# Kernel optimization log

Measured on AMD Instinct MI355X. Metric: run time of the kernel, lower is better.

Reference implementation:

```python
import jax, jax.numpy as jnp
import numpy as np


def _dwconv_silu(feat, w, b):
    # feat: (B, L, C); depthwise 1D conv, kernel 7, pad 3, then SiLU (PointLiteConv)
    x = jnp.swapaxes(feat, 1, 2)  # (B, C, L)
    y = jax.lax.conv_general_dilated(x, w, (1,), [(3, 3)],
                                     feature_group_count=x.shape[1],
                                     dimension_numbers=('NCH', 'OIH', 'NCH'))
    y = y + b[None, :, None]
    return jnp.swapaxes(jax.nn.silu(y), 1, 2)


def _issm_scan(x, h0, dt, A, Bm, Cm, Dp):
    # x: (B,L,H,P)  h0: (B,H,P,N)  dt: (B,L,H,N)  A: (H,1)  Bm,Cm: (B,L,1,N)  Dp: (H,)
    dA = jnp.exp(dt * A)                      # (B,L,H,N) discrete decay
    u = dt * Bm                               # (B,L,H,N) input coeff (ngroups=1 broadcast)
    Cb = jnp.broadcast_to(Cm, dt.shape)       # (B,L,H,N)

    def step(h, inp):
        dA_t, u_t, x_t, c_t = inp             # (B,H,N),(B,H,N),(B,H,P),(B,H,N)
        h = dA_t[:, :, None, :] * h + x_t[..., None] * u_t[:, :, None, :]
        return h, jnp.einsum('bhpn,bhn->bhp', h, c_t)

    xs = tuple(jnp.moveaxis(a, 1, 0) for a in (dA, u, x, Cb))
    hF, ys = jax.lax.scan(step, h0, xs)
    y = jnp.moveaxis(ys, 0, 1) + Dp[None, None, :, None] * x
    return y, hF


def setup_inputs() -> dict:
    key = jax.random.key(0)
    ks = jax.random.split(key, 20)
    B, L, K = 2, 2048, 64
    d_model, d_state, d_dist, H, G, d_inner = 512, 64, 4, 8, 1, 1024
    c_conv = d_inner + 2 * G  # 1026
    s = 0.02
    dt0 = jnp.exp(jax.random.uniform(ks[12], (H,)) * (np.log(0.1) - np.log(1e-4)) + np.log(1e-4))
    dt0 = jnp.clip(dt0, 1e-4, None)
    return {
        'in_key': jax.random.normal(ks[0], (B, L, d_model), jnp.float32),
        'in_query': jax.random.normal(ks[1], (B, K, d_model), jnp.float32),
        'dist': jax.random.uniform(ks[2], (B, L, K, d_dist), jnp.float32),
        'key_xyz': jax.random.normal(ks[3], (B, L, 3), jnp.float32),
        'key_proj_w': jax.random.normal(ks[4], (2 * d_inner + 2 * G + H, d_model), jnp.float32) * s,
        'key_conv_w': jax.random.normal(ks[5], (c_conv, 1, 7), jnp.float32) * s,
        'key_conv_b': jnp.zeros((c_conv,), jnp.float32),
        'key_conv_back_w': jax.random.normal(ks[6], (c_conv, 1, 7), jnp.float32) * s,
        'key_conv_back_b': jnp.zeros((c_conv,), jnp.float32),
        'query_proj_w': jax.random.normal(ks[7], (d_inner, d_model), jnp.float32) * s,
        'bc_proj_w': jax.random.normal(ks[8], (2 * G, d_dist), jnp.float32) * s,
        'dt_proj_w': jax.random.normal(ks[9], (H, d_dist), jnp.float32) * s,
        'dt_bias': dt0 + jnp.log(-jnp.expm1(-dt0)),
        'A_log': jnp.log(jax.random.uniform(ks[10], (H,), jnp.float32, 1.0, 16.0)),
        'D_param': jnp.ones((H,), jnp.float32),
        'out_key_w': jax.random.normal(ks[11], (d_model, d_inner), jnp.float32) * s,
        'out_query_w': jax.random.normal(ks[13], (d_model, d_inner), jnp.float32) * s,
        'key_norm_w': jnp.ones((d_inner,), jnp.float32),
        'q_ln_w': jnp.ones((d_inner,), jnp.float32),
        'q_ln_b': jnp.zeros((d_inner,), jnp.float32),
    }


def reference(in_key, in_query, dist, key_xyz, key_proj_w, key_conv_w, key_conv_b,
              key_conv_back_w, key_conv_back_b, query_proj_w, bc_proj_w, dt_proj_w,
              dt_bias, A_log, D_param, out_key_w, out_query_w, key_norm_w, q_ln_w, q_ln_b):
    B, L, _ = in_key.shape
    K = in_query.shape[1]
    d_inner = query_proj_w.shape[0]
    H = dt_bias.shape[0]
    G = bc_proj_w.shape[0] // 2
    P = d_inner // H

    zxbcdt = in_key @ key_proj_w.T                       # (B,L,2*di+2G+H)
    z = zxbcdt[..., :d_inner]
    xbc = zxbcdt[..., d_inner:2 * d_inner + 2 * G]
    dt_head = zxbcdt[..., 2 * d_inner + 2 * G:]          # (B,L,H)

    xbc_f = _dwconv_silu(xbc, key_conv_w, key_conv_b)
    x = xbc_f[..., :d_inner]
    b_bias = xbc_f[..., d_inner:d_inner + G]
    c_bias = xbc_f[..., d_inner + G:]
    xbc_b = _dwconv_silu(xbc, key_conv_back_w, key_conv_back_b)
    x_bk = xbc_b[..., :d_inner]
    b_bias_b = xbc_b[..., d_inner:d_inner + G]
    c_bias_b = xbc_b[..., d_inner + G:]

    # initial state: 'b l (h hd) -> b h hd l'  -> (B,H,P,K)
    h0 = (in_query @ query_proj_w.T).reshape(B, K, H, P).transpose(0, 2, 3, 1)
    A = -jnp.exp(A_log)[:, None]                         # (H,1), repeated over d_state

    bc = dist @ bc_proj_w.T                              # (B,L,K,2G)
    b_base = jnp.swapaxes(bc[..., :G], -1, -2)           # (B,L,G,K)
    c_base = jnp.swapaxes(bc[..., G:], -1, -2)
    Bm = b_base + b_bias[..., None]
    Cm = c_base + c_bias[..., None]
    Bmb = b_base + b_bias_b[..., None]
    Cmb = c_base + c_bias_b[..., None]

    dt = jax.nn.softplus(jnp.swapaxes(dist @ dt_proj_w.T, -1, -2)
                         + dt_head[..., None] + dt_bias[None, None, :, None])  # (B,L,H,K)

    xh = x.reshape(B, L, H, P)
    y_f, h_f = _issm_scan(xh, h0, dt, A, Bm, Cm, D_param)
    xb = jnp.flip(x_bk.reshape(B, L, H, P), 1)
    y_b, h_b = _issm_scan(xb, h0, jnp.flip(dt, 1), A, jnp.flip(Bmb, 1), jnp.flip(Cmb, 1), D_param)
    y = (y_f + jnp.flip(y_b, 1)) * 0.5                   # (B,L,H,P)
    h_last = (h_f + h_b) * 0.5                           # (B,H,P,K)

    key_feat = y.reshape(B, L, d_inner)
    xg = key_feat * jax.nn.silu(z)                       # gated RMSNorm (gate before norm)
    key_n = xg * jax.lax.rsqrt(jnp.mean(xg * xg, -1, keepdims=True) + 1e-5) * key_norm_w
    out_key = key_n @ out_key_w.T

    q = h_last.transpose(0, 3, 1, 2).reshape(B, K, d_inner)  # 'b h p l -> b l (h p)'
    mu = jnp.mean(q, -1, keepdims=True)
    var = jnp.mean((q - mu) ** 2, -1, keepdims=True)
    qn = (q - mu) * jax.lax.rsqrt(var + 1e-5) * q_ln_w + q_ln_b
    out_query = qn @ out_query_w.T
    return out_key, out_query
```

## Files before the change

kernel.cpp:

```cpp
#include <hip/hip_runtime.h>
#include <hip/hip_bf16.h>
#include <cstdint>

constexpr int B_ = 2, L_ = 2048, K_ = 64, H_ = 8, P_ = 128, DI = 1024;
constexpr int NPROJ = 2058;
constexpr int NC = L_ / 64;
constexpr int XBCS = 1040;

typedef unsigned short u16;
typedef short bf16x8 __attribute__((ext_vector_type(8)));
typedef float f32x4 __attribute__((ext_vector_type(4)));

__constant__ int c_sz[20] = {2097152,65536,1048576,12288,1053696,7182,1026,7182,1026,
                             524288,8,32,8,8,8,524288,524288,1024,1024,1024};
__constant__ int c_of[20] = {16,2097168,2162704,3211280,3223568,4277264,4284446,4285472,
                             4292654,4293680,4817968,4817976,4818008,4818016,4818024,
                             4818032,5342320,5866608,5867632,5868656};
constexpr int TOT_IN = 5869664;
constexpr int OF_INKEY = 16, OF_INQ = 2097168, OF_DIST = 2162704, OF_KPW = 3223568;
constexpr int OF_CONVW = 4277264, OF_CONVB = 4284446, OF_CONVBW = 4285472, OF_CONVBB = 4292654;
constexpr int OF_QPW = 4293680, OF_BCW = 4817968, OF_DTW = 4817976, OF_DTBIAS = 4818008;
constexpr int OF_ALOG = 4818016, OF_D = 4818024, OF_OKW = 4818032, OF_OQW = 5342320;
constexpr int OF_KNW = 5866608, OF_QLW = 5867632, OF_QLB = 5868656;
constexpr int SEG_A = 2097152, SEG_W = 2176*512, SEG_O = 524288;
// ... 33 lines not shown
    uint2 u = *(const uint2*)p;
    float4 r;
    r.x = __uint_as_float(u.x << 16);
    r.y = __uint_as_float(u.x & 0xffff0000u);
    r.z = __uint_as_float(u.y << 16);
    r.w = __uint_as_float(u.y & 0xffff0000u);
    return r;
}
DEV float4 b2f4u(uint2 u) {
    float4 r;
    r.x = __uint_as_float(u.x << 16);
    r.y = __uint_as_float(u.x & 0xffff0000u);
    r.z = __uint_as_float(u.y << 16);
    r.w = __uint_as_float(u.y & 0xffff0000u);
    return r;
}
DEV uint2 pku2(float4 v) {
    uint2 u;
    u.x = (unsigned)f2b(v.x) | ((unsigned)f2b(v.y) << 16);
    u.y = (unsigned)f2b(v.z) | ((unsigned)f2b(v.w) << 16);
    return u;
}
DEV void st4b(u16* p, float4 v) { *(uint2*)p = pku2(v); }
DEV unsigned pk2(float a, float b) { return (unsigned)f2b(a) | ((unsigned)f2b(b) << 16); }

#define GLL16(gp, lp) __builtin_amdgcn_global_load_lds( \
    (const __attribute__((address_space(1))) unsigned int*)(gp), \
    (__attribute__((address_space(3))) unsigned int*)(lp), 16, 0, 0)

struct SrcPtrs { const void* p[20]; };

__global__ void k_sentinel(float* out) { out[threadIdx.x] = 1e9f; }

DEV u16 cvt_elem(const void* p, int idx, bool bf) {
    if (bf) return ((const u16*)p)[idx];
    return f2b(((const float*)p)[idx]);
}
__global__ __launch_bounds__(256) void k_stage(SrcPtrs sp, float* ws) {
    int g = blockIdx.x * 256 + threadIdx.x;
    bool bf = (((const u16*)sp.p[17])[0] == 0x3F80u);
    if (g < TOT_IN) {
        int seg = 0, rem = g;
        while (rem >= c_sz[seg]) { rem -= c_sz[seg]; ++seg; }
        if (seg == 0 || seg == 1 || seg == 4 || seg == 9 || seg == 15 || seg == 16) return;
        float v;
        if (bf) v = b2f(((const u16*)sp.p[seg])[rem]);
        else    v = ((const float*)sp.p[seg])[rem];
// ... 37 lines not shown
    #pragma unroll
    for (int i = 0; i < 4; ++i)
        #pragma unroll
        for (int j = 0; j < 4; ++j) acc[i][j] = zero4;
    for (int kt = 0; kt < 512; kt += 32) {
        __syncthreads();
        GLL16(Ab + (size_t)(m0 + srow)*512      + kt + scol, As + (w*512));
        GLL16(Ab + (size_t)(m0 + 64 + srow)*512 + kt + scol, As + (2048 + w*512));
        GLL16(Wb + (size_t)(n0 + srow)*512      + kt + scol, Bs + (w*512));
        GLL16(Wb + (size_t)(n0 + 64 + srow)*512 + kt + scol, Bs + (2048 + w*512));
        __syncthreads();
        bf16x8 af[4], bfr[4];
        #pragma unroll
        for (int mi = 0; mi < 4; ++mi) af[mi]  = *(const bf16x8*)&As[(wm*64 + mi*16 + lr)*32 + lq*8];
        #pragma unroll
        for (int ni = 0; ni < 4; ++ni) bfr[ni] = *(const bf16x8*)&Bs[(wn*64 + ni*16 + lr)*32 + lq*8];
        #pragma unroll
        for (int mi = 0; mi < 4; ++mi)
            #pragma unroll
            for (int ni = 0; ni < 4; ++ni)
                acc[mi][ni] = __builtin_amdgcn_mfma_f32_16x16x32_bf16(af[mi], bfr[ni], acc[mi][ni], 0, 0, 0);
    }
    u16* xbc = (u16*)(ws + WXBC);
    #pragma unroll
    for (int mi = 0; mi < 4; ++mi)
        #pragma unroll
        for (int ni = 0; ni < 4; ++ni)
            #pragma unroll
            for (int r = 0; r < 4; ++r) {
                int m = m0 + wm*64 + mi*16 + lq*4 + r;
                int n = n0 + wn*64 + ni*16 + lr;
                if (n >= NPROJ) continue;
                float v = acc[mi][ni][r];
                if (n < 1024)       ws[WZ + m*1024 + n] = v;
                else if (n < 2050)  xbc[m*XBCS + (n-1024)] = f2b(v);
                else                ws[WDTH + m*8 + (n-2050)] = v;
            }
}

__global__ __launch_bounds__(256) void k_conv(float* ws) {
    int tile = blockIdx.x;
    int bl0 = tile * 16;
    int l0 = bl0 & (L_ - 1);
    int base = bl0 - l0;
    int cb = blockIdx.y, tid = threadIdx.x;
    int cch = cb * 256 + tid;
    if (cb == 4) { if (tid >= 2) return; cch = 1024 + tid; }
    const u16* xbc = (const u16*)(ws + WXBC);
    const float* wfp = ws + OF_CONVW + cch*7;
    const float* wbp = ws + OF_CONVBW + cch*7;
    float wf[7], wb[7];
    #pragma unroll
    for (int j = 0; j < 7; ++j) { wf[j] = wfp[j]; wb[j] = wbp[j]; }
    float bfv = ws[OF_CONVB + cch], bbv = ws[OF_CONVBB + cch];
    float win[22];
    #pragma unroll
    for (int j = 0; j < 22; ++j) {
        int l2 = l0 - 3 + j;
        win[j] = (l2 >= 0 && l2 < L_) ? b2f(xbc[(base + l2)*XBCS + cch]) : 0.f;
    }
    u16* XF = (u16*)(ws + WXF);
    u16* XB = (u16*)(ws + WXBK);
    #pragma unroll
    for (int i = 0; i < 16; ++i) {
        float af = bfv, ab = bbv;
        #pragma unroll
        for (int j = 0; j < 7; ++j) { af += win[i+j]*wf[j]; ab += win[i+j]*wb[j]; }
        af = silu_(af); ab = silu_(ab);
        if (cb < 4) {
            XF[(bl0 + i)*1024 + cch] = f2b(af);
            XB[(bl0 + i)*1024 + cch] = f2b(ab);
        } else if (cch == 1024) {
            ws[WBBF + bl0 + i] = af; ws[WBBB + bl0 + i] = ab;
        } else {
            ws[WCBF + bl0 + i] = af; ws[WCBB + bl0 + i] = ab;
        }
    }
}

__global__ __launch_bounds__(256) void k_dtbc(float* ws) {
    int g = blockIdx.x * 256 + threadIdx.x;
    if (g >= B_*L_*K_) return;
    int k = g & 63, bl = g >> 6;
    float4 d4 = ld4(&ws[OF_DIST + g*4]);
    const float* bcw = ws + OF_BCW;
    ws[WBBASE + g] = d4.x*bcw[0] + d4.y*bcw[1] + d4.z*bcw[2] + d4.w*bcw[3];
    ws[WCBASE + g] = d4.x*bcw[4] + d4.y*bcw[5] + d4.z*bcw[6] + d4.w*bcw[7];
    const float* dtw = ws + OF_DTW;
    const float* dtb = ws + OF_DTBIAS;
    const float* dth = ws + WDTH + bl*8;
    #pragma unroll
    for (int h = 0; h < 8; ++h) {
        float t = d4.x*dtw[h*4] + d4.y*dtw[h*4+1] + d4.z*dtw[h*4+2] + d4.w*dtw[h*4+3]
                + dth[h] + dtb[h];
        float sp = (t > 20.f) ? t : log1pf(__expf(t));
        ws[WDT + (bl*8 + h)*64 + k] = sp;
    }
}

__global__ __launch_bounds__(256) void k_h0mm(float* ws) {
    __shared__ u16 As[128*32], Bs[128*32];
    const u16* Ab = (const u16*)(ws + OF_INQ);
    const u16* Wb = (const u16*)(ws + OF_QPW);
    int tid = threadIdx.x, w = tid >> 6, l = tid & 63;
    int n0 = blockIdx.x * 128;
    int wm = w & 1, wn = w >> 1;
    int lr = l & 15, lq = l >> 4;
    int srow = tid >> 2, scol = (tid & 3) * 8;
    f32x4 zero4 = {0.f, 0.f, 0.f, 0.f};
    f32x4 acc[4][4];
    #pragma unroll
    for (int i = 0; i < 4; ++i)
        #pragma unroll
        for (int j = 0; j < 4; ++j) acc[i][j] = zero4;
    for (int kt = 0; kt < 512; kt += 32) {
        __syncthreads();
        GLL16(Ab + (size_t)(srow)*512      + kt + scol, As + (w*512));
        GLL16(Ab + (size_t)(64 + srow)*512 + kt + scol, As + (2048 + w*512));
        GLL16(Wb + (size_t)(n0 + srow)*512      + kt + scol, Bs + (w*512));
        GLL16(Wb + (size_t)(n0 + 64 + srow)*512 + kt + scol, Bs + (2048 + w*512));
        __syncthreads();
        bf16x8 af[4], bfr[4];
        #pragma unroll
        for (int mi = 0; mi < 4; ++mi) af[mi]  = *(const bf16x8*)&As[(wm*64 + mi*16 + lr)*32 + lq*8];
        #pragma unroll
        for (int ni = 0; ni < 4; ++ni) bfr[ni] = *(const bf16x8*)&Bs[(wn*64 + ni*16 + lr)*32 + lq*8];
        #pragma unroll
        for (int mi = 0; mi < 4; ++mi)
            #pragma unroll
            for (int ni = 0; ni < 4; ++ni)
                acc[mi][ni] = __builtin_amdgcn_mfma_f32_16x16x32_bf16(af[mi], bfr[ni], acc[mi][ni], 0, 0, 0);
    }
    #pragma unroll
    for (int mi = 0; mi < 4; ++mi)
        #pragma unroll
        for (int ni = 0; ni < 4; ++ni)
            #pragma unroll
            for (int r = 0; r < 4; ++r) {
                int m = wm*64 + mi*16 + lq*4 + r;
                int n = n0 + wn*64 + ni*16 + lr;
                int b = m >> 6, kq = m & 63, h = n >> 7, p = n & 127;
                ws[WH0I + ((b*8 + h)*64 + kq)*128 + p] = acc[mi][ni][r];
            }
}

__global__ __launch_bounds__(256, 3) void k_scanA(float* ws) {
    __shared__ float scs[4096];
    __shared__ u16 sUeD[64*72];
    __shared__ u16 sCe[64*72];
    __shared__ u16 sM[64*72];
    __shared__ u16 sUeO[32*72];
    __shared__ float sG[128];
    u16* sXt = (u16*)scs;
    int bx = blockIdx.x;
    int c = bx & 31, dir = (bx >> 5) & 1, h = (bx >> 6) & 7, b = bx >> 9;
    int tid = threadIdx.x, w = tid >> 6, l = tid & 63;
    int lr = l & 15, tq = l >> 4;
    float Ah = -__expf(ws[OF_ALOG + h]);
    float Dv = ws[OF_D + h];
    const float* dt = ws + WDT;
    const float* bbase = ws + WBBASE; const float* cbase = ws + WCBASE;
    const float* bbias = ws + (dir ? WBBB : WBBF);
    const float* cbias = ws + (dir ? WCBB : WCBF);
    for (int q = tid; q < 1024; q += 256) {
        int t = q >> 4, k4 = (q & 15) << 2;
        int gt = dir ? (L_ - 1 - (c*64 + t)) : (c*64 + t);
// ... 59 lines not shown
                bf16x8 a  = *(const bf16x8*)&sCe[(ttile*16 + lr)*72 + kh*32 + tq*8];
                bf16x8 bb = *(const bf16x8*)&Bb [(stile*16 + lr)*72 + kh*32 + tq*8];
                acc = __builtin_amdgcn_mfma_f32_16x16x32_bf16(a, bb, acc, 0, 0, 0);
            }
            #pragma unroll
            for (int r = 0; r < 4; ++r) {
                int row = ttile*16 + tq*4 + r, col = stile*16 + lr;
                sM[row*72 + col] = f2b(row >= col ? acc[r] : 0.f);
            }
        }
    }
    __syncthreads();
    for (int q = tid; q < 4096; q += 256) {
        int k = q >> 6, s = q & 63;
        sCe[k*72 + s] = f2b(b2f(sUeD[s*72 + k]) * sG[((s >> 5) << 6) + k]);
    }
    __syncthreads();
    bf16x8 aM[2], aU[2];
    #pragma unroll
    for (int kh = 0; kh < 2; ++kh) {
        aM[kh] = *(const bf16x8*)&sM [(w*16 + lr)*72 + kh*32 + tq*8];
        aU[kh] = *(const bf16x8*)&sCe[(w*16 + lr)*72 + kh*32 + tq*8];
    }
    float* yloc = ws + (dir ? WYB : WYF);
    const u16* Xsrc = (const u16*)(ws + (dir ? WXBK : WXF));
    u16* DH = (u16*)(ws + WDH);
    int bhd = (b*8 + h)*2 + dir;
    for (int ph = 0; ph < 2; ++ph) {
        #pragma unroll
        for (int g3 = 0; g3 < 2; ++g3) {
            int t0 = w*16 + g3*8;
            u16 x[8];
            #pragma unroll
            for (int j = 0; j < 8; ++j) {
                int row = c*64 + t0 + j;
                int gt = dir ? (L_ - 1 - row) : row;
                x[j] = Xsrc[(b*L_ + gt)*1024 + h*128 + ph*64 + l];
            }
            uint4 qv;
            qv.x = (unsigned)x[0] | ((unsigned)x[1] << 16);
            qv.y = (unsigned)x[2] | ((unsigned)x[3] << 16);
            qv.z = (unsigned)x[4] | ((unsigned)x[5] << 16);
            qv.w = (unsigned)x[6] | ((unsigned)x[7] << 16);
            *(uint4*)&sXt[l*72 + t0] = qv;
        }
        __syncthreads();
        f32x4 accY[4], accD[4];
        #pragma unroll
        for (int pi = 0; pi < 4; ++pi) { accY[pi] = {0.f,0.f,0.f,0.f}; accD[pi] = {0.f,0.f,0.f,0.f}; }
        #pragma unroll
        for (int pi = 0; pi < 4; ++pi) {
            bf16x8 bX0 = *(const bf16x8*)&sXt[(pi*16 + lr)*72 +  0 + tq*8];
            bf16x8 bX1 = *(const bf16x8*)&sXt[(pi*16 + lr)*72 + 32 + tq*8];
            accY[pi] = __builtin_amdgcn_mfma_f32_16x16x32_bf16(aM[0], bX0, accY[pi], 0, 0, 0);
            accY[pi] = __builtin_amdgcn_mfma_f32_16x16x32_bf16(aM[1], bX1, accY[pi], 0, 0, 0);
            accD[pi] = __builtin_amdgcn_mfma_f32_16x16x32_bf16(aU[0], bX0, accD[pi], 0, 0, 0);
            accD[pi] = __builtin_amdgcn_mfma_f32_16x16x32_bf16(aU[1], bX1, accD[pi], 0, 0, 0);
        }
        #pragma unroll
        for (int pi = 0; pi < 4; ++pi) {
            int p = pi*16 + lr;
            #pragma unroll
            for (int r = 0; r < 4; ++r) {
                int t = w*16 + tq*4 + r;
                int gt = dir ? (L_ - 1 - (c*64 + t)) : (c*64 + t);
                float xv = b2f(sXt[p*72 + t]);
                yloc[(b*L_ + gt)*1024 + h*128 + ph*64 + p] = accY[pi][r] + Dv*xv;
                int ks = w*16 + tq*4 + r;
                DH[(size_t)((bhd*32 + c)*64 + ks)*128 + ph*64 + p] = f2b(accD[pi][r]);
            }
        }
        __syncthreads();
    }
}

__global__ __launch_bounds__(256) void k_carry(float* ws) {
    int bx = blockIdx.x;
    int pg = bx & 7, dir = (bx >> 3) & 1, h = (bx >> 4) & 7, b = bx >> 7;
    int tid = threadIdx.x;
    int k = tid >> 2, p = pg*16 + (tid & 3)*4;
    int bhd = (b*8 + h)*2 + dir;
    float ear[NC];
    const float* Eb = ws + WE + bhd*32*64 + k;
    #pragma unroll
    for (int c = 0; c < NC; ++c) ear[c] = Eb[c*64];
    float4 hr = ld4(&ws[WH0I + ((b*8 + h)*64 + k)*128 + p]);
    u16* DH = (u16*)(ws + WDH);
    size_t base0 = (size_t)(bhd*32*64 + k)*128 + p;
    uint2 dbuf[4];
    #pragma unroll
    for (int i = 0; i < 4; ++i) dbuf[i] = *(const uint2*)&DH[base0 + (size_t)i*8192];
    #pragma unroll
    for (int c = 0; c < NC; ++c) {
        float4 d = b2f4u(dbuf[c & 3]);
        *(uint2*)&DH[base0 + (size_t)c*8192] = pku2(hr);
        if (c + 4 < NC) dbuf[c & 3] = *(const uint2*)&DH[base0 + (size_t)(c + 4)*8192];
        float e = ear[c];
        hr.x = e*hr.x + d.x; hr.y = e*hr.y + d.y; hr.z = e*hr.z + d.z; hr.w = e*hr.w + d.w;
    }
    st4(&ws[WHFIN + (bhd*64 + k)*128 + p], hr);
}

__global__ __launch_bounds__(256, 3) void k_scanB(float* ws) {
    __shared__ float scs[4096];
    __shared__ u16 sCf[64*72], sCb[64*72];
    __shared__ u16 sHf[64*72], sHb[64*72];
    int bx = blockIdx.x;
    int j = bx & 31, h = (bx >> 5) & 7, b = bx >> 8;
    int tid = threadIdx.x, w = tid >> 6, l = tid & 63;
    int lr = l & 15, tq = l >> 4;
    float Ah = -__expf(ws[OF_ALOG + h]);
    for (int q = tid; q < 1024; q += 256) {
        int t = q >> 4, k4 = (q & 15) << 2;
        int bl = b*L_ + j*64 + t;
        float4 dv = ld4(&ws[WDT + (bl*8 + h)*64 + k4]);
        st4(&scs[t*64 + k4], make_float4(dv.x*Ah, dv.y*Ah, dv.z*Ah, dv.w*Ah));
    }
    __syncthreads();
    {
        float* tmp = (float*)sCf;
        int kk = tid & 63, seg = tid >> 6;
        float run = 0.f;
        for (int t = seg*16; t < seg*16 + 16; ++t) { run += scs[t*64 + kk]; scs[t*64 + kk] = run; }
        tmp[seg*64 + kk] = run;
        __syncthreads();
        float off = 0.f;
        for (int s2 = 0; s2 < seg; ++s2) off += tmp[s2*64 + kk];
        __syncthreads();
        if (seg > 0)
            for (int t = seg*16; t < seg*16 + 16; ++t) scs[t*64 + kk] += off;
    }
    __syncthreads();
    for (int q = tid; q < 4096; q += 256) {
        int t = q >> 6, k = q & 63;
        int bl = b*L_ + j*64 + t;
        float pref = scs[t*64 + k];
        float prev = (t == 0) ? 0.f : scs[(t-1)*64 + k];
        float tot  = scs[63*64 + k];
        float cb0 = ws[WCBASE + bl*64 + k];
        sCf[t*72 + k] = f2b((cb0 + ws[WCBF + bl]) * __expf(pref));
        sCb[t*72 + k] = f2b((cb0 + ws[WCBB + bl]) * __expf(tot - prev));
    }
    const u16* h0f = (const u16*)(ws + WDH) + (size_t)((((b*8 + h)*2 + 0)*32 + j)*64)*128;
    const u16* h0b = (const u16*)(ws + WDH) + (size_t)((((b*8 + h)*2 + 1)*32 + (31 - j))*64)*128;
    __syncthreads();
    bf16x8 af[2], ab_[2];
    #pragma unroll
    for (int kh = 0; kh < 2; ++kh) {
        af[kh]  = *(const bf16x8*)&sCf[(w*16 + lr)*72 + kh*32 + tq*8];
        ab_[kh] = *(const bf16x8*)&sCb[(w*16 + lr)*72 + kh*32 + tq*8];
    }
    u16* xgb = (u16*)(ws + WXF);
    for (int ph = 0; ph < 2; ++ph) {
        #pragma unroll
        for (int g2 = 0; g2 < 2; ++g2) {
            int k0 = w*16 + g2*8;
            u16 xf[8], xb[8];
            #pragma unroll
            for (int jj = 0; jj < 8; ++jj) {
                xf[jj] = h0f[(k0 + jj)*128 + ph*64 + l];
                xb[jj] = h0b[(k0 + jj)*128 + ph*64 + l];
            }
            uint4 qf, qb;
            qf.x = (unsigned)xf[0] | ((unsigned)xf[1] << 16);
            qf.y = (unsigned)xf[2] | ((unsigned)xf[3] << 16);
            qf.z = (unsigned)xf[4] | ((unsigned)xf[5] << 16);
            qf.w = (unsigned)xf[6] | ((unsigned)xf[7] << 16);
            qb.x = (unsigned)xb[0] | ((unsigned)xb[1] << 16);
            qb.y = (unsigned)xb[2] | ((unsigned)xb[3] << 16);
            qb.z = (unsigned)xb[4] | ((unsigned)xb[5] << 16);
            qb.w = (unsigned)xb[6] | ((unsigned)xb[7] << 16);
            *(uint4*)&sHf[l*72 + k0] = qf;
            *(uint4*)&sHb[l*72 + k0] = qb;
        }
        __syncthreads();
        f32x4 accf[4], accb[4];
        #pragma unroll
        for (int pi = 0; pi < 4; ++pi) { accf[pi] = {0.f,0.f,0.f,0.f}; accb[pi] = {0.f,0.f,0.f,0.f}; }
        #pragma unroll
        for (int pi = 0; pi < 4; ++pi) {
            bf16x8 bf0 = *(const bf16x8*)&sHf[(pi*16 + lr)*72 +  0 + tq*8];
            bf16x8 bf1 = *(const bf16x8*)&sHf[(pi*16 + lr)*72 + 32 + tq*8];
            bf16x8 bb0 = *(const bf16x8*)&sHb[(pi*16 + lr)*72 +  0 + tq*8];
            bf16x8 bb1 = *(const bf16x8*)&sHb[(pi*16 + lr)*72 + 32 + tq*8];
            accf[pi] = __builtin_amdgcn_mfma_f32_16x16x32_bf16(af[0],  bf0, accf[pi], 0, 0, 0);
            accf[pi] = __builtin_amdgcn_mfma_f32_16x16x32_bf16(af[1],  bf1, accf[pi], 0, 0, 0);
            accb[pi] = __builtin_amdgcn_mfma_f32_16x16x32_bf16(ab_[0], bb0, accb[pi], 0, 0, 0);
            accb[pi] = __builtin_amdgcn_mfma_f32_16x16x32_bf16(ab_[1], bb1, accb[pi], 0, 0, 0);
        }
        #pragma unroll
        for (int pi = 0; pi < 4; ++pi) {
            int p = pi*16 + lr;
            #pragma unroll
            for (int r = 0; r < 4; ++r) {
                int t = w*16 + tq*4 + r;
                int off = (b*L_ + j*64 + t)*1024 + h*128 + ph*64 + p;
                float yf = ws[WYF + off], yb = ws[WYB + off], zv = ws[WZ + off];
                float o = 0.5f*(yf + yb + accf[pi][r] + accb[pi][r]) * silu_(zv);
                xgb[off] = f2b(o);
            }
        }
        __syncthreads();
    }
}

__global__ __launch_bounds__(256) void k_rms(float* ws) {
    __shared__ float red[4];
    __shared__ float sstat;
    int row = blockIdx.x;
    const u16* xg = (const u16*)(ws + WXF) + row*1024;
    float4 v = b2f4(&xg[threadIdx.x*4]);
    float ss = v.x*v.x + v.y*v.y + v.z*v.z + v.w*v.w;
    #pragma unroll
    for (int o = 32; o > 0; o >>= 1) ss += __shfl_down(ss, o);
    if ((threadIdx.x & 63) == 0) red[threadIdx.x >> 6] = ss;
    __syncthreads();
    if (threadIdx.x == 0) {
        float t = red[0] + red[1] + red[2] + red[3];
        sstat = rsqrtf(t * (1.f/1024.f) + 1e-5f);
    }
    __syncthreads();
    float sr = sstat;
    float4 kw = ld4(&ws[OF_KNW + threadIdx.x*4]);
// ... 27 lines not shown
        for (int ni = 0; ni < 2; ++ni) bfr[ni] = *(const bf16x8*)&Bs[(wn*32 + ni*16 + lr)*32 + lq*8];
        #pragma unroll
        for (int mi = 0; mi < 4; ++mi)
            #pragma unroll
            for (int ni = 0; ni < 2; ++ni)
                acc[mi][ni] = __builtin_amdgcn_mfma_f32_16x16x32_bf16(af[mi], bfr[ni], acc[mi][ni], 0, 0, 0);
    }
    bool bf = (((const u16*)in17)[0] == 0x3F80u);
    #pragma unroll
    for (int mi = 0; mi < 4; ++mi)
        #pragma unroll
        for (int ni = 0; ni < 2; ++ni)
            #pragma unroll
            for (int r = 0; r < 4; ++r) {
                int m = m0 + wm*64 + mi*16 + lq*4 + r;
                int n = n0 + wn*32 + ni*16 + lr;
                int idx = m*512 + n;
                float v = acc[mi][ni][r];
                if (bf) ((__hip_bfloat16*)d_out)[idx] = __float2bfloat16(v);
                else    ((float*)d_out)[idx] = v;
            }
}

__global__ __launch_bounds__(256) void k_queryLN(float* ws) {
    __shared__ float sq[1024];
    __shared__ float red1[4], red2[4], sstat[2];
    int bk = blockIdx.x;
    int b = bk >> 6, kq = bk & 63;
    int tid = threadIdx.x;
    for (int i = tid; i < 1024; i += 256) {
        int h = i >> 7, p = i & 127;
        int i0 = (((b*8 + h)*2 + 0)*64 + kq)*128 + p;
        int i1 = (((b*8 + h)*2 + 1)*64 + kq)*128 + p;
        sq[i] = 0.5f * (ws[WHFIN + i0] + ws[WHFIN + i1]);
    }
    __syncthreads();
    float4 v = ld4(&sq[tid*4]);
    float s1 = v.x + v.y + v.z + v.w;
    float s2 = v.x*v.x + v.y*v.y + v.z*v.z + v.w*v.w;
    #pragma unroll
    for (int o = 32; o > 0; o >>= 1) { s1 += __shfl_down(s1, o); s2 += __shfl_down(s2, o); }
    if ((tid & 63) == 0) { red1[tid >> 6] = s1; red2[tid >> 6] = s2; }
    __syncthreads();
    if (tid == 0) {
        float S1 = red1[0]+red1[1]+red1[2]+red1[3];
        float S2 = red2[0]+red2[1]+red2[2]+red2[3];
        float mu = S1 * (1.f/1024.f);
        float var = S2 * (1.f/1024.f) - mu*mu;
        sstat[0] = mu; sstat[1] = rsqrtf(var + 1e-5f);
    }
    __syncthreads();
    float mu = sstat[0], rs = sstat[1];
    u16* qn = (u16*)(ws + WXBC);
    float4 kw = ld4(&ws[OF_QLW + tid*4]);
    float4 kb = ld4(&ws[OF_QLB + tid*4]);
    st4b(qn + bk*1024 + tid*4,
         make_float4((v.x - mu)*rs*kw.x + kb.x, (v.y - mu)*rs*kw.y + kb.y,
                     (v.z - mu)*rs*kw.z + kb.z, (v.w - mu)*rs*kw.w + kb.w));
}

__global__ __launch_bounds__(256) void k_queryMM(float* ws, void* d_out, const void* in17) {
    __shared__ u16 As[128*32], Bs[128*32];
    const u16* Ab = (const u16*)(ws + WXBC);
    const u16* Wb = (const u16*)(ws + OF_OQW);
    int tid = threadIdx.x, w = tid >> 6, l = tid & 63;
    int n0 = blockIdx.x * 128;
    int wm = w & 1, wn = w >> 1;
    int lr = l & 15, lq = l >> 4;
    int srow = tid >> 2, scol = (tid & 3) * 8;
    f32x4 zero4 = {0.f, 0.f, 0.f, 0.f};
    f32x4 acc[4][4];
    #pragma unroll
    for (int i = 0; i < 4; ++i)
        #pragma unroll
        for (int jj = 0; jj < 4; ++jj) acc[i][jj] = zero4;
    for (int kt = 0; kt < 1024; kt += 32) {
        __syncthreads();
        GLL16(Ab + (size_t)(srow)*1024      + kt + scol, As + (w*512));
        GLL16(Ab + (size_t)(64 + srow)*1024 + kt + scol, As + (2048 + w*512));
        GLL16(Wb + (size_t)(n0 + srow)*1024      + kt + scol, Bs + (w*512));
        GLL16(Wb + (size_t)(n0 + 64 + srow)*1024 + kt + scol, Bs + (2048 + w*512));
        __syncthreads();
        bf16x8 af[4], bfr[4];
        #pragma unroll
        for (int mi = 0; mi < 4; ++mi) af[mi]  = *(const bf16x8*)&As[(wm*64 + mi*16 + lr)*32 + lq*8];
        #pragma unroll
        for (int ni = 0; ni < 4; ++ni) bfr[ni] = *(const bf16x8*)&Bs[(wn*64 + ni*16 + lr)*32 + lq*8];
        #pragma unroll
        for (int mi = 0; mi < 4; ++mi)
            #pragma unroll
            for (int ni = 0; ni < 4; ++ni)
                acc[mi][ni] = __builtin_amdgcn_mfma_f32_16x16x32_bf16(af[mi], bfr[ni], acc[mi][ni], 0, 0, 0);
    }
    bool bf = (((const u16*)in17)[0] == 0x3F80u);
    #pragma unroll
    for (int mi = 0; mi < 4; ++mi)
        #pragma unroll
        for (int ni = 0; ni < 4; ++ni)
            #pragma unroll
            for (int r = 0; r < 4; ++r) {
                int m = wm*64 + mi*16 + lq*4 + r;
                int n = n0 + wn*64 + ni*16 + lr;
                if (n >= 512) continue;
                int idx = 2097152 + m*512 + n;
                float v = acc[mi][ni][r];
                if (bf) ((__hip_bfloat16*)d_out)[idx] = __float2bfloat16(v);
                else    ((float*)d_out)[idx] = v;
            }
}

extern "C" void kernel_launch(void* const* d_in, const int* in_sizes, int n_in,
                              void* d_out, int out_size, void* d_ws, size_t ws_size,
                              hipStream_t stream) {
    float* ws = (float*)d_ws;
    if (ws_size < (size_t)WEND * sizeof(float)) {
        k_sentinel<<<1, 64, 0, stream>>>((float*)d_out);
        return;
    }
    SrcPtrs sp;
    for (int i = 0; i < 20; ++i) sp.p[i] = d_in[i];
    k_stage<<<(TOT_IN + NCAST + 255)/256, 256, 0, stream>>>(sp, ws);
    k_gemm_proj<<<dim3(17, 32), 256, 0, stream>>>(ws);
    k_conv<<<dim3(B_*L_/16, 5), 256, 0, stream>>>(ws);
    k_dtbc<<<(B_*L_*K_)/256, 256, 0, stream>>>(ws);
    k_h0mm<<<8, 256, 0, stream>>>(ws);
    k_scanA<<<1024, 256, 0, stream>>>(ws);
    k_carry<<<256, 256, 0, stream>>>(ws);
    k_scanB<<<512, 256, 0, stream>>>(ws);
    k_rms<<<4096, 256, 0, stream>>>(ws);
    k_outkey<<<dim3(8, 32), 256, 0, stream>>>(ws, d_out, d_in[17]);
    k_queryLN<<<128, 256, 0, stream>>>(ws);
    k_queryMM<<<4, 256, 0, stream>>>(ws, d_out, d_in[17]);
}
```

Measured before the change: 332.4 us.

## Fuse mid-stage kernels, store z and y as bf16, stage scan stores through LDS

Merges conv, dt/BC, and h0 GEMM into one launch. Folds the query LayerNorm and query GEMM into extra blocks of scanB. Stores z and the scan outputs as bf16 instead of fp32, which halves that traffic. Scan outputs and the gating epilogue now go through swizzled LDS so global stores and loads are 16-byte coalesced. This cuts launch count and memory traffic, at the cost of extra barriers and lower precision for the intermediates.

Result: slower. 362.4 us (+9.0%).

```diff
diff --git a/kernel.cpp b/kernel.cpp
--- a/kernel.cpp
+++ b/kernel.cpp
@@ -79,7 +79,6 @@
     return u;
 }
 DEV void st4b(u16* p, float4 v) { *(uint2*)p = pku2(v); }
-DEV unsigned pk2(float a, float b) { return (unsigned)f2b(a) | ((unsigned)f2b(b) << 16); }
 
 #define GLL16(gp, lp) __builtin_amdgcn_global_load_lds( \
     (const __attribute__((address_space(1))) unsigned int*)(gp), \
@@ -163,6 +162,7 @@
                 acc[mi][ni] = __builtin_amdgcn_mfma_f32_16x16x32_bf16(af[mi], bfr[ni], acc[mi][ni], 0, 0, 0);
     }
     u16* xbc = (u16*)(ws + WXBC);
+    u16* zb  = (u16*)(ws + WZ);
     #pragma unroll
     for (int mi = 0; mi < 4; ++mi)
         #pragma unroll
@@ -173,116 +173,117 @@
                 int n = n0 + wn*64 + ni*16 + lr;
                 if (n >= NPROJ) continue;
                 float v = acc[mi][ni][r];
-                if (n < 1024)       ws[WZ + m*1024 + n] = v;
+                if (n < 1024)       zb[m*1024 + n] = f2b(v);
                 else if (n < 2050)  xbc[m*XBCS + (n-1024)] = f2b(v);
                 else                ws[WDTH + m*8 + (n-2050)] = v;
             }
 }
 
-__global__ __launch_bounds__(256) void k_conv(float* ws) {
-    int tile = blockIdx.x;
-    int bl0 = tile * 16;
-    int l0 = bl0 & (L_ - 1);
-    int base = bl0 - l0;
-    int cb = blockIdx.y, tid = threadIdx.x;
-    int cch = cb * 256 + tid;
-    if (cb == 4) { if (tid >= 2) return; cch = 1024 + tid; }
-    const u16* xbc = (const u16*)(ws + WXBC);
-    const float* wfp = ws + OF_CONVW + cch*7;
-    const float* wbp = ws + OF_CONVBW + cch*7;
-    float wf[7], wb[7];
-    #pragma unroll
-    for (int j = 0; j < 7; ++j) { wf[j] = wfp[j]; wb[j] = wbp[j]; }
-    float bfv = ws[OF_CONVB + cch], bbv = ws[OF_CONVBB + cch];
-    float win[22];
-    #pragma unroll
-    for (int j = 0; j < 22; ++j) {
-        int l2 = l0 - 3 + j;
-        win[j] = (l2 >= 0 && l2 < L_) ? b2f(xbc[(base + l2)*XBCS + cch]) : 0.f;
-    }
-    u16* XF = (u16*)(ws + WXF);
-    u16* XB = (u16*)(ws + WXBK);
-    #pragma unroll
-    for (int i = 0; i < 16; ++i) {
-        float af = bfv, ab = bbv;
-        #pragma unroll
-        for (int j = 0; j < 7; ++j) { af += win[i+j]*wf[j]; ab += win[i+j]*wb[j]; }
-        af = silu_(af); ab = silu_(ab);
-        if (cb < 4) {
-            XF[(bl0 + i)*1024 + cch] = f2b(af);
-            XB[(bl0 + i)*1024 + cch] = f2b(ab);
-        } else if (cch == 1024) {
-            ws[WBBF + bl0 + i] = af; ws[WBBB + bl0 + i] = ab;
-        } else {
-            ws[WCBF + bl0 + i] = af; ws[WCBB + bl0 + i] = ab;
-        }
-    }
-}
-
-__global__ __launch_bounds__(256) void k_dtbc(float* ws) {
-    int g = blockIdx.x * 256 + threadIdx.x;
-    if (g >= B_*L_*K_) return;
-    int k = g & 63, bl = g >> 6;
-    float4 d4 = ld4(&ws[OF_DIST + g*4]);
-    const float* bcw = ws + OF_BCW;
-    ws[WBBASE + g] = d4.x*bcw[0] + d4.y*bcw[1] + d4.z*bcw[2] + d4.w*bcw[3];
-    ws[WCBASE + g] = d4.x*bcw[4] + d4.y*bcw[5] + d4.z*bcw[6] + d4.w*bcw[7];
-    const float* dtw = ws + OF_DTW;
-    const float* dtb = ws + OF_DTBIAS;
-    const float* dth = ws + WDTH + bl*8;
-    #pragma unroll
-    for (int h = 0; h < 8; ++h) {
-        float t = d4.x*dtw[h*4] + d4.y*dtw[h*4+1] + d4.z*dtw[h*4+2] + d4.w*dtw[h*4+3]
-                + dth[h] + dtb[h];
-        float sp = (t > 20.f) ? t : log1pf(__expf(t));
-        ws[WDT + (bl*8 + h)*64 + k] = sp;
-    }
-}
-
-__global__ __launch_bounds__(256) void k_h0mm(float* ws) {
+__global__ __launch_bounds__(256) void k_mid(float* ws) {
     __shared__ u16 As[128*32], Bs[128*32];
-    const u16* Ab = (const u16*)(ws + OF_INQ);
-    const u16* Wb = (const u16*)(ws + OF_QPW);
-    int tid = threadIdx.x, w = tid >> 6, l = tid & 63;
-    int n0 = blockIdx.x * 128;
-    int wm = w & 1, wn = w >> 1;
-    int lr = l & 15, lq = l >> 4;
-    int srow = tid >> 2, scol = (tid & 3) * 8;
-    f32x4 zero4 = {0.f, 0.f, 0.f, 0.f};
-    f32x4 acc[4][4];
-    #pragma unroll
-    for (int i = 0; i < 4; ++i)
-        #pragma unroll
-        for (int j = 0; j < 4; ++j) acc[i][j] = zero4;
-    for (int kt = 0; kt < 512; kt += 32) {
-        __syncthreads();
-        GLL16(Ab + (size_t)(srow)*512      + kt + scol, As + (w*512));
-        GLL16(Ab + (size_t)(64 + srow)*512 + kt + scol, As + (2048 + w*512));
-        GLL16(Wb + (size_t)(n0 + srow)*512      + kt + scol, Bs + (w*512));
-        GLL16(Wb + (size_t)(n0 + 64 + srow)*512 + kt + scol, Bs + (2048 + w*512));
-        __syncthreads();
-        bf16x8 af[4], bfr[4];
-        #pragma unroll
-        for (int mi = 0; mi < 4; ++mi) af[mi]  = *(const bf16x8*)&As[(wm*64 + mi*16 + lr)*32 + lq*8];
-        #pragma unroll
-        for (int ni = 0; ni < 4; ++ni) bfr[ni] = *(const bf16x8*)&Bs[(wn*64 + ni*16 + lr)*32 + lq*8];
+    int bx = blockIdx.x, tid = threadIdx.x;
+    if (bx < 1280) {
+        int cb = bx >> 8, tile = bx & 255;
+        int bl0 = tile * 16;
+        int l0 = bl0 & (L_ - 1);
+        int base = bl0 - l0;
+        int cch = cb * 256 + tid;
+        if (cb == 4) { if (tid >= 2) return; cch = 1024 + tid; }
+        const u16* xbc = (const u16*)(ws + WXBC);
+        const float* wfp = ws + OF_CONVW + cch*7;
+        const float* wbp = ws + OF_CONVBW + cch*7;
+        float wf[7], wb[7];
+        #pragma unroll
+        for (int j = 0; j < 7; ++j) { wf[j] = wfp[j]; wb[j] = wbp[j]; }
+        float bfv = ws[OF_CONVB + cch], bbv = ws[OF_CONVBB + cch];
+        float win[22];
+        #pragma unroll
+        for (int j = 0; j < 22; ++j) {
+            int l2 = l0 - 3 + j;
+            win[j] = (l2 >= 0 && l2 < L_) ? b2f(xbc[(base + l2)*XBCS + cch]) : 0.f;
+        }
+        u16* XF = (u16*)(ws + WXF);
+        u16* XB = (u16*)(ws + WXBK);
+        #pragma unroll
+        for (int i = 0; i < 16; ++i) {
+            float af = bfv, ab = bbv;
+            #pragma unroll
+            for (int j = 0; j < 7; ++j) { af += win[i+j]*wf[j]; ab += win[i+j]*wb[j]; }
+            af = silu_(af); ab = silu_(ab);
+            if (cb < 4) {
+                XF[(bl0 + i)*1024 + cch] = f2b(af);
+                XB[(bl0 + i)*1024 + cch] = f2b(ab);
+            } else if (cch == 1024) {
+                ws[WBBF + bl0 + i] = af; ws[WBBB + bl0 + i] = ab;
+            } else {
+                ws[WCBF + bl0 + i] = af; ws[WCBB + bl0 + i] = ab;
+            }
+        }
+        return;
+    }
+    if (bx < 2304) {
+        int g = (bx - 1280) * 256 + tid;
+        int k = g & 63, bl = g >> 6;
+        float4 d4 = ld4(&ws[OF_DIST + g*4]);
+        const float* bcw = ws + OF_BCW;
+        ws[WBBASE + g] = d4.x*bcw[0] + d4.y*bcw[1] + d4.z*bcw[2] + d4.w*bcw[3];
+        ws[WCBASE + g] = d4.x*bcw[4] + d4.y*bcw[5] + d4.z*bcw[6] + d4.w*bcw[7];
+        const float* dtw = ws + OF_DTW;
+        const float* dtb = ws + OF_DTBIAS;
+        const float* dth = ws + WDTH + bl*8;
+        #pragma unroll
+        for (int h = 0; h < 8; ++h) {
+            float t = d4.x*dtw[h*4] + d4.y*dtw[h*4+1] + d4.z*dtw[h*4+2] + d4.w*dtw[h*4+3]
+                    + dth[h] + dtb[h];
+            float sp = (t > 20.f) ? t : log1pf(__expf(t));
+            ws[WDT + (bl*8 + h)*64 + k] = sp;
+        }
+        return;
+    }
+    {
+        const u16* Ab = (const u16*)(ws + OF_INQ);
+        const u16* Wb = (const u16*)(ws + OF_QPW);
+        int w = tid >> 6, l = tid & 63;
+        int n0 = (bx - 2304) * 128;
+        int wm = w & 1, wn = w >> 1;
+        int lr = l & 15, lq = l >> 4;
+        int srow = tid >> 2, scol = (tid & 3) * 8;
+        f32x4 zero4 = {0.f, 0.f, 0.f, 0.f};
+        f32x4 acc[4][4];
+        #pragma unroll
+        for (int i = 0; i < 4; ++i)
+            #pragma unroll
+            for (int j = 0; j < 4; ++j) acc[i][j] = zero4;
+        for (int kt = 0; kt < 512; kt += 32) {
+            __syncthreads();
+            GLL16(Ab + (size_t)(srow)*512      + kt + scol, As + (w*512));
+            GLL16(Ab + (size_t)(64 + srow)*512 + kt + scol, As + (2048 + w*512));
+            GLL16(Wb + (size_t)(n0 + srow)*512      + kt + scol, Bs + (w*512));
+            GLL16(Wb + (size_t)(n0 + 64 + srow)*512 + kt + scol, Bs + (2048 + w*512));
+            __syncthreads();
+            bf16x8 af[4], bfr[4];
+            #pragma unroll
+            for (int mi = 0; mi < 4; ++mi) af[mi]  = *(const bf16x8*)&As[(wm*64 + mi*16 + lr)*32 + lq*8];
+            #pragma unroll
+            for (int ni = 0; ni < 4; ++ni) bfr[ni] = *(const bf16x8*)&Bs[(wn*64 + ni*16 + lr)*32 + lq*8];
+            #pragma unroll
+            for (int mi = 0; mi < 4; ++mi)
+                #pragma unroll
+                for (int ni = 0; ni < 4; ++ni)
+                    acc[mi][ni] = __builtin_amdgcn_mfma_f32_16x16x32_bf16(af[mi], bfr[ni], acc[mi][ni], 0, 0, 0);
+        }
         #pragma unroll
         for (int mi = 0; mi < 4; ++mi)
             #pragma unroll
             for (int ni = 0; ni < 4; ++ni)
-                acc[mi][ni] = __builtin_amdgcn_mfma_f32_16x16x32_bf16(af[mi], bfr[ni], acc[mi][ni], 0, 0, 0);
-    }
-    #pragma unroll
-    for (int mi = 0; mi < 4; ++mi)
-        #pragma unroll
-        for (int ni = 0; ni < 4; ++ni)
-            #pragma unroll
-            for (int r = 0; r < 4; ++r) {
-                int m = wm*64 + mi*16 + lq*4 + r;
-                int n = n0 + wn*64 + ni*16 + lr;
-                int b = m >> 6, kq = m & 63, h = n >> 7, p = n & 127;
-                ws[WH0I + ((b*8 + h)*64 + kq)*128 + p] = acc[mi][ni][r];
-            }
+                #pragma unroll
+                for (int r = 0; r < 4; ++r) {
+                    int m = wm*64 + mi*16 + lq*4 + r;
+                    int n = n0 + wn*64 + ni*16 + lr;
+                    int b = m >> 6, kq = m & 63, h = n >> 7, p = n & 127;
+                    ws[WH0I + ((b*8 + h)*64 + kq)*128 + p] = acc[mi][ni][r];
+                }
+    }
 }
 
 __global__ __launch_bounds__(256, 3) void k_scanA(float* ws) {
@@ -388,7 +389,10 @@
         aM[kh] = *(const bf16x8*)&sM [(w*16 + lr)*72 + kh*32 + tq*8];
         aU[kh] = *(const bf16x8*)&sCe[(w*16 + lr)*72 + kh*32 + tq*8];
     }
-    float* yloc = ws + (dir ? WYB : WYF);
+    __syncthreads();
+    u16* sYst = sM;
+    u16* sDst = sCe;
+    u16* yloc16 = (u16*)(ws + (dir ? WYB : WYF));
     const u16* Xsrc = (const u16*)(ws + (dir ? WXBK : WXF));
     u16* DH = (u16*)(ws + WDH);
     int bhd = (b*8 + h)*2 + dir;
@@ -429,12 +433,26 @@
             #pragma unroll
             for (int r = 0; r < 4; ++r) {
                 int t = w*16 + tq*4 + r;
-                int gt = dir ? (L_ - 1 - (c*64 + t)) : (c*64 + t);
                 float xv = b2f(sXt[p*72 + t]);
-                yloc[(b*L_ + gt)*1024 + h*128 + ph*64 + p] = accY[pi][r] + Dv*xv;
-                int ks = w*16 + tq*4 + r;
-                DH[(size_t)((bhd*32 + c)*64 + ks)*128 + ph*64 + p] = f2b(accD[pi][r]);
-            }
+                sYst[t*64 + (((pi + t) & 3) << 4) + lr] = f2b(accY[pi][r] + Dv*xv);
+                sDst[t*64 + (((pi + t) & 3) << 4) + lr] = f2b(accD[pi][r]);
+            }
+        }
+        __syncthreads();
+        {
+            int t2 = tid >> 2, cg = tid & 3;
+            int swz = ((cg + t2) & 3) << 4;
+            int gt2 = dir ? (L_ - 1 - (c*64 + t2)) : (c*64 + t2);
+            uint4 y0 = *(uint4*)&sYst[t2*64 + swz];
+            uint4 d0 = *(uint4*)&sDst[t2*64 + swz];
+            u16* yp = yloc16 + (size_t)(b*L_ + gt2)*1024 + h*128 + ph*64 + cg*16;
+            u16* dp = DH + (size_t)((bhd*32 + c)*64 + t2)*128 + ph*64 + cg*16;
+            *(uint4*)yp = y0;
+            *(uint4*)dp = d0;
+            uint4 y1 = *(uint4*)&sYst[t2*64 + swz + 8];
+            uint4 d1 = *(uint4*)&sDst[t2*64 + swz + 8];
+            *(uint4*)(yp + 8) = y1;
+            *(uint4*)(dp + 8) = d1;
         }
         __syncthreads();
     }
@@ -467,13 +485,108 @@
     st4(&ws[WHFIN + (bhd*64 + k)*128 + p], hr);
 }
 
-__global__ __launch_bounds__(256, 3) void k_scanB(float* ws) {
+__global__ __launch_bounds__(256, 3) void k_scanB(float* ws, void* d_out, const void* in17) {
     __shared__ float scs[4096];
     __shared__ u16 sCf[64*72], sCb[64*72];
     __shared__ u16 sHf[64*72], sHb[64*72];
     int bx = blockIdx.x;
+    int tid = threadIdx.x;
+    bool bf16out = (((const u16*)in17)[0] == 0x3F80u);
+    if (bx >= 512) {
+        int n0 = (bx - 512) * 128;
+        u16* As = (u16*)scs;
+        u16* Bs = (u16*)scs + 4096;
+        float* smu = (float*)sCf;
+        float* srs = smu + 128;
+        {
+            int m = tid >> 1, halfsel = tid & 1;
+            int b = m >> 6, kq = m & 63;
+            float s1 = 0.f, s2 = 0.f;
+            for (int i = halfsel*512; i < halfsel*512 + 512; i += 4) {
+                int h2 = i >> 7, p = i & 127;
+                float4 hf = ld4(&ws[WHFIN + ((((b*8 + h2)*2 + 0)*64 + kq)*128 + p)]);
+                float4 hb = ld4(&ws[WHFIN + ((((b*8 + h2)*2 + 1)*64 + kq)*128 + p)]);
+                float qx = 0.5f*(hf.x+hb.x), qy = 0.5f*(hf.y+hb.y);
+                float qz = 0.5f*(hf.z+hb.z), qw = 0.5f*(hf.w+hb.w);
+                s1 += qx+qy+qz+qw;
+                s2 += qx*qx+qy*qy+qz*qz+qw*qw;
+            }
+            s1 += __shfl_xor(s1, 1); s2 += __shfl_xor(s2, 1);
+            if (halfsel == 0) {
+                float mu = s1 * (1.f/1024.f);
+                float var = s2 * (1.f/1024.f) - mu*mu;
+                smu[m] = mu; srs[m] = rsqrtf(var + 1e-5f);
+            }
+        }
+        __syncthreads();
+        const u16* Wb = (const u16*)(ws + OF_OQW);
+        int w = tid >> 6, l = tid & 63;
+        int wm = w & 1, wn = w >> 1, lr = l & 15, lq = l >> 4;
+        int srow = tid >> 2, scol = (tid & 3) * 8;
+        f32x4 acc[4][4];
+        #pragma unroll
+        for (int i = 0; i < 4; ++i)
+            #pragma unroll
+            for (int j = 0; j < 4; ++j) acc[i][j] = {0.f,0.f,0.f,0.f};
+        int m2 = tid >> 1, csel = (tid & 1) * 16;
+        int b2 = m2 >> 6, kq2 = m2 & 63;
+        float mu2 = smu[m2], rs2 = srs[m2];
+        for (int kt = 0; kt < 1024; kt += 32) {
+            __syncthreads();
+            GLL16(Wb + (size_t)(n0 + srow)*1024      + kt + scol, Bs + (w*512));
+            GLL16(Wb + (size_t)(n0 + 64 + srow)*1024 + kt + scol, Bs + (2048 + w*512));
+            {
+                int i0 = kt + csel;
+                int h2 = i0 >> 7, p0 = i0 & 127;
+                const float* hfp = ws + WHFIN + ((((b2*8 + h2)*2 + 0)*64 + kq2)*128 + p0);
+                const float* hbp = ws + WHFIN + ((((b2*8 + h2)*2 + 1)*64 + kq2)*128 + p0);
+                uint2 pk[4];
+                #pragma unroll
+                for (int j4 = 0; j4 < 4; ++j4) {
+                    float4 hf = ld4(hfp + j4*4);
+                    float4 hb = ld4(hbp + j4*4);
+                    float4 kw = ld4(&ws[OF_QLW + i0 + j4*4]);
+                    float4 kb = ld4(&ws[OF_QLB + i0 + j4*4]);
+                    float4 qn;
+                    qn.x = (0.5f*(hf.x+hb.x) - mu2)*rs2*kw.x + kb.x;
+                    qn.y = (0.5f*(hf.y+hb.y) - mu2)*rs2*kw.y + kb.y;
+                    qn.z = (0.5f*(hf.z+hb.z) - mu2)*rs2*kw.z + kb.z;
+                    qn.w = (0.5f*(hf.w+hb.w) - mu2)*rs2*kw.w + kb.w;
+                    pk[j4] = pku2(qn);
+                }
+                *(uint4*)&As[m2*32 + csel]     = make_uint4(pk[0].x, pk[0].y, pk[1].x, pk[1].y);
+                *(uint4*)&As[m2*32 + csel + 8] = make_uint4(pk[2].x, pk[2].y, pk[3].x, pk[3].y);
+            }
+            __syncthreads();
+            bf16x8 af[4], bfr[4];
+            #pragma unroll
+            for (int mi = 0; mi < 4; ++mi) af[mi]  = *(const bf16x8*)&As[(wm*64 + mi*16 + lr)*32 + lq*8];
+            #pragma unroll
+            for (int ni = 0; ni < 4; ++ni) bfr[ni] = *(const bf16x8*)&Bs[(wn*64 + ni*16 + lr)*32 + lq*8];
+            #pragma unroll
+            for (int mi = 0; mi < 4; ++mi)
+                #pragma unroll
+                for (int ni = 0; ni < 4; ++ni)
+                    acc[mi][ni] = __builtin_amdgcn_mfma_f32_16x16x32_bf16(af[mi], bfr[ni], acc[mi][ni], 0, 0, 0);
+        }
+        #pragma unroll
+        for (int mi = 0; mi < 4; ++mi)
+            #pragma unroll
+            for (int ni = 0; ni < 4; ++ni)
+                #pragma unroll
+                for (int r = 0; r < 4; ++r) {
+                    int m = wm*64 + mi*16 + lq*4 + r;
+                    int n = n0 + wn*64 + ni*16 + lr;
+                    if (n >= 512) continue;
+                    int idx = 2097152 + m*512 + n;
+                    float v = acc[mi][ni][r];
+                    if (bf16out) ((__hip_bfloat16*)d_out)[idx] = __float2bfloat16(v);
+                    else         ((float*)d_out)[idx] = v;
+                }
+        return;
+    }
     int j = bx & 31, h = (bx >> 5) & 7, b = bx >> 8;
-    int tid = threadIdx.x, w = tid >> 6, l = tid & 63;
+    int w = tid >> 6, l = tid & 63;
     int lr = l & 15, tq = l >> 4;
     float Ah = -__expf(ws[OF_ALOG + h]);
     for (int q = tid; q < 1024; q += 256) {
@@ -516,7 +629,14 @@
         af[kh]  = *(const bf16x8*)&sCf[(w*16 + lr)*72 + kh*32 + tq*8];
         ab_[kh] = *(const bf16x8*)&sCb[(w*16 + lr)*72 + kh*32 + tq*8];
     }
+    const u16* yf16 = (const u16*)(ws + WYF);
+    const u16* yb16 = (const u16*)(ws + WYB);
+    const u16* zb   = (const u16*)(ws + WZ);
     u16* xgb = (u16*)(ws + WXF);
+    u16* sYf = sCf;
+    u16* sYb = sCb;
+    u16* sZ  = sHf;
+    u16* sO  = sHb;
     for (int ph = 0; ph < 2; ++ph) {
         #pragma unroll
         for (int g2 = 0; g2 < 2; ++g2) {
@@ -554,17 +674,42 @@
             accb[pi] = __builtin_amdgcn_mfma_f32_16x16x32_bf16(ab_[0], bb0, accb[pi], 0, 0, 0);
             accb[pi] = __builtin_amdgcn_mfma_f32_16x16x32_bf16(ab_[1], bb1, accb[pi], 0, 0, 0);
         }
+        __syncthreads();
+        {
+            int t2 = tid >> 2, cg = tid & 3;
+            int swz = ((cg + t2) & 3) << 4;
+            size_t off = (size_t)(b*L_ + j*64 + t2)*1024 + h*128 + ph*64 + cg*16;
+            uint4 a0 = *(const uint4*)(yf16 + off);
+            uint4 a1 = *(const uint4*)(yf16 + off + 8);
+            uint4 b0 = *(const uint4*)(yb16 + off);
+            uint4 b1 = *(const uint4*)(yb16 + off + 8);
+            uint4 c0 = *(const uint4*)(zb + off);
+            uint4 c1 = *(const uint4*)(zb + off + 8);
+            *(uint4*)&sYf[t2*64 + swz] = a0; *(uint4*)&sYf[t2*64 + swz + 8] = a1;
+            *(uint4*)&sYb[t2*64 + swz] = b0; *(uint4*)&sYb[t2*64 + swz + 8] = b1;
+            *(uint4*)&sZ [t2*64 + swz] = c0; *(uint4*)&sZ [t2*64 + swz + 8] = c1;
+        }
+        __syncthreads();
         #pragma unroll
         for (int pi = 0; pi < 4; ++pi) {
-            int p = pi*16 + lr;
             #pragma unroll
             for (int r = 0; r < 4; ++r) {
                 int t = w*16 + tq*4 + r;
-                int off = (b*L_ + j*64 + t)*1024 + h*128 + ph*64 + p;
-                float yf = ws[WYF + off], yb = ws[WYB + off], zv = ws[WZ + off];
+                int sidx = t*64 + (((pi + t) & 3) << 4) + lr;
+                float yf = b2f(sYf[sidx]), yb = b2f(sYb[sidx]), zv = b2f(sZ[sidx]);
                 float o = 0.5f*(yf + yb + accf[pi][r] + accb[pi][r]) * silu_(zv);
-                xgb[off] = f2b(o);
-            }
+                sO[sidx] = f2b(o);
+            }
+        }
+        __syncthreads();
+        {
+            int t2 = tid >> 2, cg = tid & 3;
+            int swz = ((cg + t2) & 3) << 4;
+            uint4 o0 = *(uint4*)&sO[t2*64 + swz];
+            uint4 o1 = *(uint4*)&sO[t2*64 + swz + 8];
+            u16* op = xgb + (size_t)(b*L_ + j*64 + t2)*1024 + h*128 + ph*64 + cg*16;
+            *(uint4*)op = o0;
+            *(uint4*)(op + 8) = o1;
         }
         __syncthreads();
     }
@@ -638,93 +783,6 @@
             }
 }
 
-__global__ __launch_bounds__(256) void k_queryLN(float* ws) {
-    __shared__ float sq[1024];
-    __shared__ float red1[4], red2[4], sstat[2];
-    int bk = blockIdx.x;
-    int b = bk >> 6, kq = bk & 63;
-    int tid = threadIdx.x;
-    for (int i = tid; i < 1024; i += 256) {
-        int h = i >> 7, p = i & 127;
-        int i0 = (((b*8 + h)*2 + 0)*64 + kq)*128 + p;
-        int i1 = (((b*8 + h)*2 + 1)*64 + kq)*128 + p;
-        sq[i] = 0.5f * (ws[WHFIN + i0] + ws[WHFIN + i1]);
-    }
-    __syncthreads();
-    float4 v = ld4(&sq[tid*4]);
-    float s1 = v.x + v.y + v.z + v.w;
-    float s2 = v.x*v.x + v.y*v.y + v.z*v.z + v.w*v.w;
-    #pragma unroll
-    for (int o = 32; o > 0; o >>= 1) { s1 += __shfl_down(s1, o); s2 += __shfl_down(s2, o); }
-    if ((tid & 63) == 0) { red1[tid >> 6] = s1; red2[tid >> 6] = s2; }
-    __syncthreads();
-    if (tid == 0) {
-        float S1 = red1[0]+red1[1]+red1[2]+red1[3];
-        float S2 = red2[0]+red2[1]+red2[2]+red2[3];
-        float mu = S1 * (1.f/1024.f);
-        float var = S2 * (1.f/1024.f) - mu*mu;
-        sstat[0] = mu; sstat[1] = rsqrtf(var + 1e-5f);
-    }
-    __syncthreads();
-    float mu = sstat[0], rs = sstat[1];
-    u16* qn = (u16*)(ws + WXBC);
-    float4 kw = ld4(&ws[OF_QLW + tid*4]);
-    float4 kb = ld4(&ws[OF_QLB + tid*4]);
-    st4b(qn + bk*1024 + tid*4,
-         make_float4((v.x - mu)*rs*kw.x + kb.x, (v.y - mu)*rs*kw.y + kb.y,
-                     (v.z - mu)*rs*kw.z + kb.z, (v.w - mu)*rs*kw.w + kb.w));
-}
-
-__global__ __launch_bounds__(256) void k_queryMM(float* ws, void* d_out, const void* in17) {
-    __shared__ u16 As[128*32], Bs[128*32];
-    const u16* Ab = (const u16*)(ws + WXBC);
-    const u16* Wb = (const u16*)(ws + OF_OQW);
-    int tid = threadIdx.x, w = tid >> 6, l = tid & 63;
-    int n0 = blockIdx.x * 128;
-    int wm = w & 1, wn = w >> 1;
-    int lr = l & 15, lq = l >> 4;
-    int srow = tid >> 2, scol = (tid & 3) * 8;
-    f32x4 zero4 = {0.f, 0.f, 0.f, 0.f};
-    f32x4 acc[4][4];
-    #pragma unroll
-    for (int i = 0; i < 4; ++i)
-        #pragma unroll
-        for (int jj = 0; jj < 4; ++jj) acc[i][jj] = zero4;
-    for (int kt = 0; kt < 1024; kt += 32) {
-        __syncthreads();
-        GLL16(Ab + (size_t)(srow)*1024      + kt + scol, As + (w*512));
-        GLL16(Ab + (size_t)(64 + srow)*1024 + kt + scol, As + (2048 + w*512));
-        GLL16(Wb + (size_t)(n0 + srow)*1024      + kt + scol, Bs + (w*512));
-        GLL16(Wb + (size_t)(n0 + 64 + srow)*1024 + kt + scol, Bs + (2048 + w*512));
-        __syncthreads();
-        bf16x8 af[4], bfr[4];
-        #pragma unroll
-        for (int mi = 0; mi < 4; ++mi) af[mi]  = *(const bf16x8*)&As[(wm*64 + mi*16 + lr)*32 + lq*8];
-        #pragma unroll
-        for (int ni = 0; ni < 4; ++ni) bfr[ni] = *(const bf16x8*)&Bs[(wn*64 + ni*16 + lr)*32 + lq*8];
-        #pragma unroll
-        for (int mi = 0; mi < 4; ++mi)
-            #pragma unroll
-            for (int ni = 0; ni < 4; ++ni)
-                acc[mi][ni] = __builtin_amdgcn_mfma_f32_16x16x32_bf16(af[mi], bfr[ni], acc[mi][ni], 0, 0, 0);
-    }
-    bool bf = (((const u16*)in17)[0] == 0x3F80u);
-    #pragma unroll
-    for (int mi = 0; mi < 4; ++mi)
-        #pragma unroll
-        for (int ni = 0; ni < 4; ++ni)
-            #pragma unroll
-            for (int r = 0; r < 4; ++r) {
-                int m = wm*64 + mi*16 + lq*4 + r;
-                int n = n0 + wn*64 + ni*16 + lr;
-                if (n >= 512) continue;
-                int idx = 2097152 + m*512 + n;
-                float v = acc[mi][ni][r];
-                if (bf) ((__hip_bfloat16*)d_out)[idx] = __float2bfloat16(v);
-                else    ((float*)d_out)[idx] = v;
-            }
-}
-
 extern "C" void kernel_launch(void* const* d_in, const int* in_sizes, int n_in,
                               void* d_out, int out_size, void* d_ws, size_t ws_size,
                               hipStream_t stream) {
@@ -737,14 +795,10 @@
     for (int i = 0; i < 20; ++i) sp.p[i] = d_in[i];
     k_stage<<<(TOT_IN + NCAST + 255)/256, 256, 0, stream>>>(sp, ws);
     k_gemm_proj<<<dim3(17, 32), 256, 0, stream>>>(ws);
-    k_conv<<<dim3(B_*L_/16, 5), 256, 0, stream>>>(ws);
-    k_dtbc<<<(B_*L_*K_)/256, 256, 0, stream>>>(ws);
-    k_h0mm<<<8, 256, 0, stream>>>(ws);
+    k_mid<<<2312, 256, 0, stream>>>(ws);
     k_scanA<<<1024, 256, 0, stream>>>(ws);
     k_carry<<<256, 256, 0, stream>>>(ws);
-    k_scanB<<<512, 256, 0, stream>>>(ws);
+    k_scanB<<<516, 256, 0, stream>>>(ws, d_out, d_in[17]);
     k_rms<<<4096, 256, 0, stream>>>(ws);
     k_outkey<<<dim3(8, 32), 256, 0, stream>>>(ws, d_out, d_in[17]);
-    k_queryLN<<<128, 256, 0, stream>>>(ws);
-    k_queryMM<<<4, 256, 0, stream>>>(ws, d_out, d_in[17]);
-}
+}
```
